# Kernel tuning notes

Measured on AMD Instinct MI355X. Metric: run time of the kernel, lower is better.

The kernel has to match this reference:

```python
import jax, jax.numpy as jnp
import numpy as np

K = 7  # kernel_size = (1, 7): horizontal cyclic shifts


@jax.custom_vjp
def binarize(x):
    # BinaryQuantizer: sign forward, clipped STE backward
    return jnp.sign(x)

def _bin_fwd(x):
    return jnp.sign(x), x

def _bin_bwd(x, g):
    # torch zeroes grad where x >= 1 or x <= -1
    return (jnp.where((x > -1.0) & (x < 1.0), g, 0.0),)

binarize.defvjp(_bin_fwd, _bin_bwd)


def setup_inputs() -> dict:
    key = jax.random.key(0)
    k1, k2, k3 = jax.random.split(key, 3)
    B, C, H, W = 32, 384, 56, 56
    x = jax.random.normal(k1, (B, C, H, W), dtype=jnp.float32)
    # weight is (out_channels, in_channels) for the 1x1 conv (squeezed kh=kw=1)
    weight = jax.random.normal(k2, (C, C), dtype=jnp.float32) * 0.05
    bias = jax.random.normal(k3, (C,), dtype=jnp.float32) * 0.01
    return {"x": x, "weight": weight, "bias": bias}


def reference(x, weight, bias):
    B, C, H, W = x.shape
    xb = binarize(x)            # sign(activations)
    wb = binarize(weight)       # sign(weights)

    # CycleFC offsets for kernel (1, K): per-channel integer horizontal shift.
    # dx_i = (i + K*1//2) % K - K//2  (gen_offset with start_idx = K//2)
    dx = (jnp.arange(C) + K // 2) % K - K // 2  # (C,) in [-K//2, K-1-K//2]

    # deform_conv2d with integer offsets == zero-padded shift:
    # shifted[b, i, h, w] = xb[b, i, h, w + dx_i], 0 if out of bounds.
    P = K
    xp = jnp.pad(xb, ((0, 0), (0, 0), (0, 0), (P, P)))
    idx = jnp.arange(W)[None, :] + dx[:, None] + P          # (C, W)
    shifted = jnp.take_along_axis(xp, idx[None, :, None, :], axis=3)  # (B,C,H,W)

    # 1x1 conv (pointwise GEMM) + bias
    out = jnp.einsum('bchw,oc->bohw', shifted, wb) + bias[None, :, None, None]
    return out
```

## Files before the change

### kernel.cpp

```cpp
#include <hip/hip_runtime.h>
#include <stdint.h>

#define B_   32
#define C_   384
#define H_   56
#define W_   56
#define HW_  (H_*W_)
#define NWORD 6


struct Masks {
    unsigned long long inv[7][NWORD];
    int nvalid[7];
};
constexpr Masks make_masks() {
    Masks m{};
    int wv[7] = {0, 1, 2, 3, 53, 54, 55};
    for (int p = 0; p < 7; ++p) {
        int nv = 0;
        for (int c = 0; c < C_; ++c) {
            int dx = (c + 3) % 7 - 3;
            int wp = wv[p] + dx;
            if (wp >= 0 && wp < W_) nv++;
            else m.inv[p][c >> 6] |= 1ull << (c & 63);
        }
        m.nvalid[p] = nv;
    }
    return m;
}
__device__ constexpr Masks MK = make_masks();

struct InvW { unsigned long long m[W_][NWORD]; };
constexpr InvW make_invw() {
    InvW t{};
    for (int w = 0; w < W_; ++w)
        for (int c = 0; c < C_; ++c) {
            int dx = (c + 3) % 7 - 3;
            int wp = w + dx;
            if (!(wp >= 0 && wp < W_)) t.m[w][c >> 6] |= 1ull << (c & 63);
        }
    return t;
}
__device__ constexpr InvW IVW = make_invw();

__global__ __launch_bounds__(64) void prep_kernel(
        const float* __restrict__ weight, const float* __restrict__ bias,
        unsigned long long* __restrict__ pw, float* __restrict__ C2) {
    int o = blockIdx.x;
    int lane = threadIdx.x;
    unsigned long long words[NWORD];
#pragma unroll
    for (int k = 0; k < NWORD; ++k) {
        float v = weight[o * C_ + k * 64 + lane];
        words[k] = __ballot(v < 0.0f);
    }
    if (lane < NWORD) pw[o * NWORD + lane] = words[lane];
    if (lane < 7) {
        int wb = 0;
#pragma unroll
        for (int k = 0; k < NWORD; ++k)
            wb += __popcll(words[k] & MK.inv[lane][k]);
        C2[o * 7 + lane] = (float)(MK.nvalid[lane] + 2 * wb) + bias[o];
    }
}

template <int K>
__device__ __forceinline__ unsigned long long pack_word(
        const float* __restrict__ xb, int w) {
    constexpr int dxt[7] = {0, 1, 2, 3, -3, -2, -1};
    unsigned long long bits = 0;
#pragma unroll
    for (int j = 0; j < 64; ++j) {
        int dx = dxt[(K * 64 + j) % 7];
        int wp = w + dx;
        int wpc = wp < 0 ? 0 : (wp > W_ - 1 ? W_ - 1 : wp);
        unsigned u = __float_as_uint(
            __builtin_nontemporal_load(&xb[(size_t)j * HW_ + wpc]));
        bits |= (unsigned long long)(u >> 31) << j;
    }
    return bits & ~IVW.m[w][K];
}

__global__ __launch_bounds__(384) void fused_kernel(
        const float* __restrict__ x,
        const unsigned long long* __restrict__ pw,
        const float* __restrict__ C2,
        float* __restrict__ out) {
    __shared__ unsigned long long xs[NWORD][W_];

    int b = blockIdx.x / H_;
    int h = blockIdx.x % H_;
    int wid  = threadIdx.x >> 6;
    int lane = threadIdx.x & 63;

    if (lane < W_) {
        const float* xb = x + ((size_t)b * C_ + wid * 64) * HW_ + h * W_;
        unsigned long long bits;
        switch (wid) {
            case 0: bits = pack_word<0>(xb, lane); break;
            case 1: bits = pack_word<1>(xb, lane); break;
            case 2: bits = pack_word<2>(xb, lane); break;
            case 3: bits = pack_word<3>(xb, lane); break;
            case 4: bits = pack_word<4>(xb, lane); break;
            default: bits = pack_word<5>(xb, lane); break;
        }
        xs[wid][lane] = bits;
    }
    __syncthreads();
    if (lane >= W_) return;

    int w = lane;
    unsigned long long xw[NWORD];
#pragma unroll
    for (int k = 0; k < NWORD; ++k)
        xw[k] = xs[k][w];

    int pat = (w < 3) ? w : ((w >= 53) ? w - 49 : 3);
    const int obase = wid * 64;
    float* op = out + ((size_t)b * C_ + obase) * HW_ + (size_t)h * W_ + w;

#pragma unroll 4
    for (int oi = 0; oi < 64; ++oi) {
        int o = obase + oi;
        const unsigned long long* wr = pw + o * NWORD;
        int U = 0;
#pragma unroll
        for (int k = 0; k < NWORD; ++k)
            U += __popcll(xw[k] ^ wr[k]);
        float v = C2[o * 7 + pat] - 2.0f * (float)U;
        __builtin_nontemporal_store(v, &op[(size_t)oi * HW_]);
    }
}

extern "C" void kernel_launch(void* const* d_in, const int* in_sizes, int n_in,
                              void* d_out, int out_size, void* d_ws, size_t ws_size,
                              hipStream_t stream) {
    const float* x      = (const float*)d_in[0];
    const float* weight = (const float*)d_in[1];
    const float* bias   = (const float*)d_in[2];
    float* out = (float*)d_out;

    unsigned long long* pw = (unsigned long long*)d_ws;
    float* C2 = (float*)((char*)d_ws + C_ * NWORD * sizeof(unsigned long long));

    prep_kernel<<<dim3(C_), dim3(64), 0, stream>>>(weight, bias, pw, C2);
    fused_kernel<<<dim3(B_ * H_), dim3(384), 0, stream>>>(x, pw, C2, out);
}
```

Measured before the change: 331.5 us.

## Replace XOR-popcount binary GEMM with bf16 MFMA on sign-encoded operands

```diff
diff --git a/kernel.cpp b/kernel.cpp
--- a/kernel.cpp
+++ b/kernel.cpp
@@ -6,129 +6,120 @@
 #define H_   56
 #define W_   56
 #define HW_  (H_*W_)
-#define NWORD 6
+#define NP_  (B_*H_*W_)
+#define PXB  128
+#define NBLK (NP_/PXB)
+#define KT_  24
+#define MT_  12
 
+typedef __attribute__((ext_vector_type(8)))  short short8;
+typedef __attribute__((ext_vector_type(16))) float float16;
 
-struct Masks {
-    unsigned long long inv[7][NWORD];
-    int nvalid[7];
-};
-constexpr Masks make_masks() {
-    Masks m{};
-    int wv[7] = {0, 1, 2, 3, 53, 54, 55};
-    for (int p = 0; p < 7; ++p) {
-        int nv = 0;
-        for (int c = 0; c < C_; ++c) {
-            int dx = (c + 3) % 7 - 3;
-            int wp = wv[p] + dx;
-            if (wp >= 0 && wp < W_) nv++;
-            else m.inv[p][c >> 6] |= 1ull << (c & 63);
-        }
-        m.nvalid[p] = nv;
-    }
-    return m;
-}
-__device__ constexpr Masks MK = make_masks();
-
-struct InvW { unsigned long long m[W_][NWORD]; };
-constexpr InvW make_invw() {
-    InvW t{};
-    for (int w = 0; w < W_; ++w)
-        for (int c = 0; c < C_; ++c) {
-            int dx = (c + 3) % 7 - 3;
-            int wp = w + dx;
-            if (!(wp >= 0 && wp < W_)) t.m[w][c >> 6] |= 1ull << (c & 63);
-        }
-    return t;
-}
-__device__ constexpr InvW IVW = make_invw();
-
-__global__ __launch_bounds__(64) void prep_kernel(
-        const float* __restrict__ weight, const float* __restrict__ bias,
-        unsigned long long* __restrict__ pw, float* __restrict__ C2) {
-    int o = blockIdx.x;
-    int lane = threadIdx.x;
-    unsigned long long words[NWORD];
+__global__ __launch_bounds__(64) void prep_w(
+        const float* __restrict__ wt, unsigned* __restrict__ wbf) {
+    int o = blockIdx.x, lane = threadIdx.x;
 #pragma unroll
-    for (int k = 0; k < NWORD; ++k) {
-        float v = weight[o * C_ + k * 64 + lane];
-        words[k] = __ballot(v < 0.0f);
-    }
-    if (lane < NWORD) pw[o * NWORD + lane] = words[lane];
-    if (lane < 7) {
-        int wb = 0;
-#pragma unroll
-        for (int k = 0; k < NWORD; ++k)
-            wb += __popcll(words[k] & MK.inv[lane][k]);
-        C2[o * 7 + lane] = (float)(MK.nvalid[lane] + 2 * wb) + bias[o];
+    for (int it = 0; it < 3; ++it) {
+        int cp = it * 64 + lane;
+        float a = wt[o * C_ + 2 * cp];
+        float b = wt[o * C_ + 2 * cp + 1];
+        unsigned ua = 0x3F80u | ((__float_as_uint(a) >> 31) << 15);
+        unsigned ub = 0x3F80u | ((__float_as_uint(b) >> 31) << 15);
+        wbf[o * (C_ / 2) + cp] = ua | (ub << 16);
     }
 }
 
-template <int K>
-__device__ __forceinline__ unsigned long long pack_word(
-        const float* __restrict__ xb, int w) {
-    constexpr int dxt[7] = {0, 1, 2, 3, -3, -2, -1};
-    unsigned long long bits = 0;
+__global__ __launch_bounds__(256, 3) void bmfma_kernel(
+        const float* __restrict__ x, const unsigned* __restrict__ wbf,
+        const float* __restrict__ bias, float* __restrict__ out) {
+    __shared__ unsigned char Bs[PXB * C_];
+
+    const int tid  = threadIdx.x;
+    const int lane = tid & 63;
+    const int wid  = tid >> 6;
+
+    const int wids  = __builtin_amdgcn_readfirstlane(wid);
+    const int cbase = wids * 96;
+
+    const int pxg0 = blockIdx.x * PXB + lane;
+    const int pxg1 = pxg0 + 64;
+    const int b0 = pxg0 / HW_, q0 = pxg0 % HW_, w0 = q0 % W_;
+    const int b1 = pxg1 / HW_, q1 = pxg1 % HW_, w1 = q1 % W_;
+    const int rowa0 = b0 * C_ * HW_ + (q0 - w0);
+    const int rowa1 = b1 * C_ * HW_ + (q1 - w1);
+    const int sw    = (lane & 15) << 1;
+
+    int cm7 = cbase % 7;
+    for (int i = 0; i < 96; i += 8) {
+        unsigned dwl[2] = {0u, 0u}, dwh[2] = {0u, 0u};
 #pragma unroll
-    for (int j = 0; j < 64; ++j) {
-        int dx = dxt[(K * 64 + j) % 7];
-        int wp = w + dx;
-        int wpc = wp < 0 ? 0 : (wp > W_ - 1 ? W_ - 1 : wp);
-        unsigned u = __float_as_uint(
-            __builtin_nontemporal_load(&xb[(size_t)j * HW_ + wpc]));
-        bits |= (unsigned long long)(u >> 31) << j;
-    }
-    return bits & ~IVW.m[w][K];
-}
-
-__global__ __launch_bounds__(384) void fused_kernel(
-        const float* __restrict__ x,
-        const unsigned long long* __restrict__ pw,
-        const float* __restrict__ C2,
-        float* __restrict__ out) {
-    __shared__ unsigned long long xs[NWORD][W_];
-
-    int b = blockIdx.x / H_;
-    int h = blockIdx.x % H_;
-    int wid  = threadIdx.x >> 6;
-    int lane = threadIdx.x & 63;
-
-    if (lane < W_) {
-        const float* xb = x + ((size_t)b * C_ + wid * 64) * HW_ + h * W_;
-        unsigned long long bits;
-        switch (wid) {
-            case 0: bits = pack_word<0>(xb, lane); break;
-            case 1: bits = pack_word<1>(xb, lane); break;
-            case 2: bits = pack_word<2>(xb, lane); break;
-            case 3: bits = pack_word<3>(xb, lane); break;
-            case 4: bits = pack_word<4>(xb, lane); break;
-            default: bits = pack_word<5>(xb, lane); break;
+        for (int j = 0; j < 8; ++j) {
+            const int c  = cbase + i + j;
+            const int dx = (cm7 < 4) ? cm7 : cm7 - 7;
+            cm7 = (cm7 == 6) ? 0 : cm7 + 1;
+            const int wp0 = w0 + dx, wp1 = w1 + dx;
+            const bool ok0 = ((unsigned)wp0 < (unsigned)W_);
+            const bool ok1 = ((unsigned)wp1 < (unsigned)W_);
+            const int wc0 = wp0 < 0 ? 0 : (wp0 > W_ - 1 ? W_ - 1 : wp0);
+            const int wc1 = wp1 < 0 ? 0 : (wp1 > W_ - 1 ? W_ - 1 : wp1);
+            const float f0 =
+                __builtin_nontemporal_load(&x[(size_t)c * HW_ + rowa0 + wc0]);
+            const float f1 =
+                __builtin_nontemporal_load(&x[(size_t)c * HW_ + rowa1 + wc1]);
+            unsigned s0 = ok0 ? ((__float_as_uint(f0) >> 31) ? 0xC0u : 0x40u) : 0u;
+            unsigned s1 = ok1 ? ((__float_as_uint(f1) >> 31) ? 0xC0u : 0x40u) : 0u;
+            dwl[j >> 2] |= s0 << ((j & 3) * 8);
+            dwh[j >> 2] |= s1 << ((j & 3) * 8);
         }
-        xs[wid][lane] = bits;
+        const int d0 = (cbase + i) >> 2;
+        *(unsigned long long*)(&Bs[lane * C_ + ((d0 ^ sw) << 2)]) =
+            (unsigned long long)dwl[0] | ((unsigned long long)dwl[1] << 32);
+        *(unsigned long long*)(&Bs[(lane + 64) * C_ + ((d0 ^ sw) << 2)]) =
+            (unsigned long long)dwh[0] | ((unsigned long long)dwh[1] << 32);
     }
     __syncthreads();
-    if (lane >= W_) return;
 
-    int w = lane;
-    unsigned long long xw[NWORD];
+    const int hl  = lane >> 5;
+    const int l31 = lane & 31;
+    const int pxl = wid * 32 + l31;
+    const int pxg = blockIdx.x * PXB + pxl;
+    const int bm  = pxg / HW_, remm = pxg % HW_;
+    const size_t outb = ((size_t)bm * C_ + hl * 4) * HW_ + remm;
+    const int swm = (pxl & 15) << 1;
+
+    short8 Bf[KT_];
 #pragma unroll
-    for (int k = 0; k < NWORD; ++k)
-        xw[k] = xs[k][w];
+    for (int kt = 0; kt < KT_; ++kt) {
+        const int d0 = kt * 4 + hl * 2;
+        unsigned long long raw = *(const unsigned long long*)(
+            &Bs[pxl * C_ + ((d0 ^ swm) << 2)]);
+        unsigned r0 = (unsigned)raw, r1 = (unsigned)(raw >> 32);
+        union { unsigned u[4]; short8 s; } uu;
+        uu.u[0] = ((r0 & 0x000000FFu) << 8) | ((r0 & 0x0000FF00u) << 16);
+        uu.u[1] = ((r0 & 0x00FF0000u) >> 8) | (r0 & 0xFF000000u);
+        uu.u[2] = ((r1 & 0x000000FFu) << 8) | ((r1 & 0x0000FF00u) << 16);
+        uu.u[3] = ((r1 & 0x00FF0000u) >> 8) | (r1 & 0xFF000000u);
+        Bf[kt] = uu.s;
+    }
 
-    int pat = (w < 3) ? w : ((w >= 53) ? w - 49 : 3);
-    const int obase = wid * 64;
-    float* op = out + ((size_t)b * C_ + obase) * HW_ + (size_t)h * W_ + w;
-
-#pragma unroll 4
-    for (int oi = 0; oi < 64; ++oi) {
-        int o = obase + oi;
-        const unsigned long long* wr = pw + o * NWORD;
-        int U = 0;
+    const unsigned* ab = wbf + l31 * (C_ / 2) + hl * 4;
+    for (int mt = 0; mt < MT_; ++mt) {
+        float16 acc = {0,0,0,0,0,0,0,0,0,0,0,0,0,0,0,0};
+        const unsigned* am = ab + mt * 32 * (C_ / 2);
 #pragma unroll
-        for (int k = 0; k < NWORD; ++k)
-            U += __popcll(xw[k] ^ wr[k]);
-        float v = C2[o * 7 + pat] - 2.0f * (float)U;
-        __builtin_nontemporal_store(v, &op[(size_t)oi * HW_]);
+        for (int kt = 0; kt < KT_; ++kt) {
+            union { uint4 v; short8 s; } av;
+            av.v = *(const uint4*)(am + kt * 8);
+            acc = __builtin_amdgcn_mfma_f32_32x32x16_bf16(av.s, Bf[kt], acc,
+                                                          0, 0, 0);
+        }
+#pragma unroll
+        for (int r = 0; r < 16; ++r) {
+            const int row = mt * 32 + (r & 3) + 8 * (r >> 2);
+            const float bv = bias[row + hl * 4];
+            __builtin_nontemporal_store(acc[r] * 0.5f + bv,
+                                        &out[outb + (size_t)row * HW_]);
+        }
     }
 }
 
@@ -140,9 +131,8 @@
     const float* bias   = (const float*)d_in[2];
     float* out = (float*)d_out;
 
-    unsigned long long* pw = (unsigned long long*)d_ws;
-    float* C2 = (float*)((char*)d_ws + C_ * NWORD * sizeof(unsigned long long));
+    unsigned* wbf = (unsigned*)d_ws;
 
-    prep_kernel<<<dim3(C_), dim3(64), 0, stream>>>(weight, bias, pw, C2);
-    fused_kernel<<<dim3(B_ * H_), dim3(384), 0, stream>>>(x, pw, C2, out);
+    prep_w<<<dim3(C_), dim3(64), 0, stream>>>(weight, wbf);
+    bmfma_kernel<<<dim3(NBLK), dim3(256), 0, stream>>>(x, wbf, bias, out);
 }
```

Result: slower. 438.0 us (+32.1%).
